# Kernel tuning notes

Measured on AMD Instinct MI355X. Metric: run time of the kernel, lower is better.

The kernel has to match this reference:

```python
import jax, jax.numpy as jnp
import numpy as np

B, C, H, W = 16, 512, 32, 32
NUM_GROUPS = 32
EPS = 1e-5


def setup_inputs() -> dict:
    key = jax.random.key(0)
    ks = jax.random.split(key, 7)
    x = jax.random.normal(ks[0], (B, C, H, W), dtype=jnp.float32)
    gamma = jnp.ones((C,), dtype=jnp.float32)
    beta = jnp.zeros((C,), dtype=jnp.float32)
    # project_in: Conv2d(C, 3C, 1) -> weight [3C, C], bias [3C]
    w_in = jax.random.normal(ks[1], (3 * C, C), dtype=jnp.float32) / np.sqrt(C)
    b_in = jnp.zeros((3 * C,), dtype=jnp.float32)
    # project_out: Conv2d(C, C, 1) with init_scale=0.0 -> zero-init in original;
    # use small random weights so gradients/outputs are non-trivial for testing.
    w_out = jax.random.normal(ks[2], (C, C), dtype=jnp.float32) / np.sqrt(C)
    b_out = jnp.zeros((C,), dtype=jnp.float32)
    return {"x": x, "gamma": gamma, "beta": beta, "w_in": w_in, "b_in": b_in,
            "w_out": w_out, "b_out": b_out}


def group_norm(x, gamma, beta):
    b, c, h, w = x.shape
    xg = x.reshape(b, NUM_GROUPS, c // NUM_GROUPS, h, w)
    mean = xg.mean(axis=(2, 3, 4), keepdims=True)
    var = xg.var(axis=(2, 3, 4), keepdims=True)
    xn = ((xg - mean) * jax.lax.rsqrt(var + EPS)).reshape(b, c, h, w)
    return xn * gamma[None, :, None, None] + beta[None, :, None, None]


def reference(x, gamma, beta, w_in, b_in, w_out, b_out):
    skip = x  # in_channels == out_channels -> Identity skip
    xn = group_norm(x, gamma, beta)
    # 1x1 conv == channel matmul
    qkv = jnp.einsum('oc,bchw->bohw', w_in, xn) + b_in[None, :, None, None]
    q, k, v = jnp.split(qkv, 3, axis=1)  # each [B, C, H, W]
    cm = q.shape[1]
    # [B, H, W, H*W] scores
    scores = jnp.einsum('bchw,bcHW->bhwHW', q, k).reshape(B, H, W, H * W)
    attn = jax.nn.softmax(scores / jnp.sqrt(jnp.float32(cm)), axis=-1)
    attn = attn.reshape(B, H, W, H, W)
    out = jnp.einsum('bhwHW,bcHW->bchw', attn, v)
    out = jnp.einsum('oc,bchw->bohw', w_out, out) + b_out[None, :, None, None]
    return out + skip
```

## Files before the change

### kernel.cpp

```cpp
#include <hip/hip_runtime.h>
#include <hip/hip_bf16.h>
#include <cstdint>
#include <cstddef>

#define HW   1024
#define NC   512
#define NB   16
#define EPSV 1e-5f

typedef __hip_bfloat16 bf16;
typedef __attribute__((ext_vector_type(8))) __bf16 bf16x8;
typedef __attribute__((ext_vector_type(4))) float f32x4;

__device__ __forceinline__ float b2f(bf16 h) { return __bfloat162float(h); }

__device__ __forceinline__ void gload16(const void* g, void* l) {
  __builtin_amdgcn_global_load_lds(
      (const __attribute__((address_space(1))) uint32_t*)g,
      (__attribute__((address_space(3))) uint32_t*)l, 16, 0, 0);
}

__global__ __launch_bounds__(256) void cvt_w_kernel(
    const float* __restrict__ wi, const float* __restrict__ wo,
    bf16* __restrict__ wib, bf16* __restrict__ wob) {
  int i = blockIdx.x * 256 + threadIdx.x;
  const float4* src;
  bf16* dst;
  int j;
  if (i < 196608) { src = (const float4*)wi; j = i; dst = wib; }
  else            { src = (const float4*)wo; j = i - 196608; dst = wob; }
  float4 v = src[j];
  union { bf16 h[4]; uint2 u; } p;
  p.h[0] = __float2bfloat16(v.x); p.h[1] = __float2bfloat16(v.y);
  p.h[2] = __float2bfloat16(v.z); p.h[3] = __float2bfloat16(v.w);
  *(uint2*)&dst[(size_t)j * 4] = p.u;
}

__global__ __launch_bounds__(256) void gn_kernel(
    const float* __restrict__ x, const float* __restrict__ gamma,
    const float* __restrict__ beta, bf16* __restrict__ xn) {
  int blk = blockIdx.x;
  int b = blk >> 5, g = blk & 31;
  size_t base = ((size_t)(b * NC + g * 16)) * HW;
  const float4* src4 = (const float4*)(x + base);
  int t = threadIdx.x;
  float s = 0.f, ss = 0.f;
  float4 v[16];
#pragma unroll
  for (int i = 0; i < 16; ++i) {
    v[i] = src4[t + i * 256];
    s  += v[i].x + v[i].y + v[i].z + v[i].w;
    ss += v[i].x * v[i].x + v[i].y * v[i].y + v[i].z * v[i].z + v[i].w * v[i].w;
  }
  __shared__ float red[256];
  red[t] = s; __syncthreads();
  for (int o = 128; o > 0; o >>= 1) { if (t < o) red[t] += red[t + o]; __syncthreads(); }
  float mean = red[0] * (1.f / 16384.f);
  __syncthreads();
  red[t] = ss; __syncthreads();
  for (int o = 128; o > 0; o >>= 1) { if (t < o) red[t] += red[t + o]; __syncthreads(); }
  float var = red[0] * (1.f / 16384.f) - mean * mean;
  float rstd = rsqrtf(var + EPSV);

  __shared__ bf16 sm[16][1032];
#pragma unroll
  for (int i = 0; i < 16; ++i) {
    int idx = t + i * 256;
    int c = idx >> 8;
    int hw4 = (idx & 255) * 4;
    float gm = gamma[g * 16 + c], bt = beta[g * 16 + c];
    union { bf16 h[4]; uint2 u; } p;
    p.h[0] = __float2bfloat16((v[i].x - mean) * rstd * gm + bt);
    p.h[1] = __float2bfloat16((v[i].y - mean) * rstd * gm + bt);
    p.h[2] = __float2bfloat16((v[i].z - mean) * rstd * gm + bt);
    p.h[3] = __float2bfloat16((v[i].w - mean) * rstd * gm + bt);
    *(uint2*)&sm[c][hw4] = p.u;
  }
  __syncthreads();
  bf16* dst = xn + (size_t)b * HW * NC + g * 16;
#pragma unroll
  for (int it = 0; it < 8; ++it) {
    int u = it * 256 + t;
    int hw = u >> 1;
    int c8 = (u & 1) * 8;
    union { bf16 h[8]; uint4 q; } p;
#pragma unroll
    for (int j = 0; j < 8; ++j) p.h[j] = sm[c8 + j][hw];
    *(uint4*)&dst[(size_t)hw * NC + c8] = p.q;
  }
}

template <int MODE>
__global__ __launch_bounds__(256) void gemm_bt(
    const bf16* __restrict__ A, int lda, long long sA,
    const bf16* __restrict__ B, int ldb, long long sB,
    void* __restrict__ Cv, int ldc, long long sC,
    int K,
    const float* __restrict__ bias) {
  __shared__ bf16 sT[2][128][32];
  int z = blockIdx.z;
  const bf16* Ab = A + (size_t)z * sA;
  const bf16* Bb = B + (size_t)z * sB;
  int n0 = blockIdx.x * 128, m0 = blockIdx.y * 128;
  int t = threadIdx.x;
  int l = t & 63, w = t >> 6;
  int wm = w >> 1, wn = w & 1;

  int srow = t >> 2;
  int scol = (t & 3) * 8;

  f32x4 acc[4][4] = {};

  const bf16* ga0 = Ab + (size_t)(m0 + srow) * lda + scol;
  const bf16* gb0 = Bb + (size_t)(n0 + srow) * ldb + scol;

  for (int k0 = 0; k0 < K; k0 += 32) {
    gload16(ga0 + k0, &sT[0][srow][scol]);
    gload16(ga0 + (size_t)64 * lda + k0, &sT[0][64 + srow][scol]);
    gload16(gb0 + k0, &sT[1][srow][scol]);
    gload16(gb0 + (size_t)64 * ldb + k0, &sT[1][64 + srow][scol]);
    __syncthreads();
    bf16x8 af[4], bfr[4];
    int kc = (l >> 4) * 8;
    int ra = wm * 64 + (l & 15);
    int rb = wn * 64 + (l & 15);
#pragma unroll
    for (int i = 0; i < 4; ++i) {
      af[i]  = *(const bf16x8*)&sT[0][ra + i * 16][kc];
      bfr[i] = *(const bf16x8*)&sT[1][rb + i * 16][kc];
    }
#pragma unroll
    for (int i = 0; i < 4; ++i)
#pragma unroll
      for (int j = 0; j < 4; ++j)
        acc[i][j] = __builtin_amdgcn_mfma_f32_16x16x32_bf16(af[i], bfr[j], acc[i][j], 0, 0, 0);
    __syncthreads();
  }

  int rbase = (l >> 4) * 4;
#pragma unroll
  for (int i = 0; i < 4; ++i) {
    int row = m0 + wm * 64 + i * 16 + rbase;
    float4 bv = make_float4(0.f, 0.f, 0.f, 0.f);
    if (MODE == 0) bv = *(const float4*)&bias[row];
    else if (MODE == 1) { if (bias) bv = *(const float4*)&bias[row]; }
#pragma unroll
    for (int j = 0; j < 4; ++j) {
      int col = n0 + wn * 64 + j * 16 + (l & 15);
      if (MODE == 0) {
        bf16* C = (bf16*)Cv + (size_t)z * sC;
        union { bf16 h[4]; uint2 u; } p;
        p.h[0] = __float2bfloat16(acc[i][j][0] + bv.x);
        p.h[1] = __float2bfloat16(acc[i][j][1] + bv.y);
        p.h[2] = __float2bfloat16(acc[i][j][2] + bv.z);
        p.h[3] = __float2bfloat16(acc[i][j][3] + bv.w);
        *(uint2*)&C[(size_t)col * ldc + row] = p.u;
      } else {
        bf16* C = (bf16*)Cv + (size_t)z * sC;
        float bb[4] = {bv.x, bv.y, bv.z, bv.w};
#pragma unroll
        for (int r = 0; r < 4; ++r)
          C[(size_t)(row + r) * ldc + col] = __float2bfloat16(acc[i][j][r] + bb[r]);
      }
    }
  }
}

__global__ __launch_bounds__(512, 1) void flash_kernel(
    const bf16* __restrict__ qk, const bf16* __restrict__ vcm,
    const bf16* __restrict__ wout, const float* __restrict__ b_out,
    const float* __restrict__ x, float* __restrict__ out) {
  __shared__ char lds[163840];
  char* Qs  = lds;
  char* Kb0 = lds + 65536;
  char* Kb1 = lds + 81920;
  char* Vs  = lds + 98304;
  char* Wb0 = lds + 65536;
  char* Wb1 = lds + 98304;
  float* redl = (float*)(lds + 131072);

  int id = blockIdx.x;
  int xcd = id & 7, rest = id >> 3;
  int q = rest & 15, bh = rest >> 4;
  int b = xcd + bh * 8;
  int i0 = q * 64;

  const char* qkC = (const char*)qk + (size_t)b * 2097152;
  const char* vC  = (const char*)vcm + (size_t)b * 1048576;
  const char* wC  = (const char*)wout;

  int t = threadIdx.x, l = t & 63, w = t >> 6;
  int l15 = l & 15, lq = l >> 4;
  int jg = w >> 1, ih = w & 1;
  int chb = w * 64;

  auto stage_k = [&](int tile_, int c_, char* dst_) {
#pragma unroll
    for (int qq = 0; qq < 2; ++qq) {
      int drow = w * 8 + qq * 4 + lq;
      int cb = l15 * 16;
      gload16(qkC + (size_t)(tile_ * 64 + drow) * 2048 + 1024 + c_ * 256
                  + (cb ^ ((drow & 7) << 4)),
              dst_ + w * 2048 + qq * 1024 + l * 16);
    }
  };
  auto stage_v = [&](int tile_, int v_) {
    int ch = v_ * 64 + w * 8 + (l >> 3);
    int cb = (l & 7) * 16;
    gload16(vC + (size_t)ch * 2048 + tile_ * 128 + (cb ^ ((ch & 7) << 4)),
            Vs + v_ * 8192 + w * 1024 + l * 16);
  };
  auto stage_w = [&](int kc_, char* dst_) {
#pragma unroll
    for (int it = 0; it < 4; ++it) {
      int idx = it * 512 + t;
      int row = idx >> 2, cb = (idx & 3) * 16;
      gload16(wC + (size_t)row * 1024 + kc_ * 64 + (cb ^ ((row & 3) << 4)),
              dst_ + idx * 16);
    }
  };

  {
    const char* qbase = qkC + (size_t)i0 * 2048;
#pragma unroll
    for (int it = 0; it < 8; ++it) {
      int s = it * 8192 + t * 16;
      int i = s >> 10, wb = s & 1023;
      gload16(qbase + (size_t)i * 2048 + (wb ^ ((i & 7) << 4)), Qs + s);
    }
  }
  stage_k(0, 0, Kb0);

  float lacc[2] = {0.f, 0.f};
  f32x4 o[4][4] = {};
  const float scl = 0.044194173824159216f;

  __syncthreads();

  for (int tile = 0; tile < 16; ++tile) {
    char* PsBuf = (tile & 1) ? Kb1 : Kb0;
    f32x4 s[2] = {};
#pragma unroll
    for (int p = 0; p < 4; ++p) {
      if (p < 3) {
        char* kd = ((p + 1 + tile) & 1) ? Kb1 : Kb0;
        stage_k(tile, p + 1, kd);
      }
      stage_v(tile, p * 2);
      stage_v(tile, p * 2 + 1);
      const char* kcur = ((p + tile) & 1) ? Kb1 : Kb0;
      int krow = jg * 16 + l15;
#pragma unroll
      for (int k2 = 0; k2 < 4; ++k2) {
        bf16x8 kf = *(const bf16x8*)(kcur + krow * 256
                      + ((k2 * 64 + lq * 16) ^ ((krow & 7) << 4)));
#pragma unroll
        for (int ni = 0; ni < 2; ++ni) {
          int i = ih * 32 + ni * 16 + l15;
          bf16x8 qf = *(const bf16x8*)(Qs + i * 1024
                        + ((p * 256 + k2 * 64 + lq * 16) ^ ((i & 7) << 4)));
          s[ni] = __builtin_amdgcn_mfma_f32_16x16x32_bf16(kf, qf, s[ni], 0, 0, 0);
        }
      }
      __syncthreads();
    }
#pragma unroll
    for (int ni = 0; ni < 2; ++ni) {
      int i = ih * 32 + ni * 16 + l15;
      float p0 = __expf(s[ni][0] * scl);
      float p1 = __expf(s[ni][1] * scl);
      float p2 = __expf(s[ni][2] * scl);
      float p3 = __expf(s[ni][3] * scl);
      lacc[ni] += p0 + p1 + p2 + p3;
      union { bf16 h[4]; uint64_t u; } pk;
      pk.h[0] = __float2bfloat16(p0); pk.h[1] = __float2bfloat16(p1);
      pk.h[2] = __float2bfloat16(p2); pk.h[3] = __float2bfloat16(p3);
      *(uint64_t*)(PsBuf + i * 128 + ((jg * 32 + lq * 8) ^ ((i & 7) << 4))) = pk.u;
    }
    __syncthreads();
    if (tile < 15) {
      char* kd = ((tile + 1) & 1) ? Kb1 : Kb0;
      stage_k(tile + 1, 0, kd);
    }
#pragma unroll
    for (int ks = 0; ks < 2; ++ks) {
      bf16x8 vf[4];
#pragma unroll
      for (int mi = 0; mi < 4; ++mi) {
        int ch = chb + mi * 16 + l15;
        vf[mi] = *(const bf16x8*)(Vs + ch * 128
                   + ((ks * 64 + lq * 16) ^ ((ch & 7) << 4)));
      }
#pragma unroll
      for (int ni = 0; ni < 4; ++ni) {
        int i = ni * 16 + l15;
        bf16x8 pf = *(const bf16x8*)(PsBuf + i * 128
                      + ((ks * 64 + lq * 16) ^ ((i & 7) << 4)));
#pragma unroll
        for (int mi = 0; mi < 4; ++mi)
          o[mi][ni] = __builtin_amdgcn_mfma_f32_16x16x32_bf16(vf[mi], pf, o[mi][ni], 0, 0, 0);
      }
    }
    __syncthreads();
  }

  stage_w(0, Wb0);
#pragma unroll
  for (int ni = 0; ni < 2; ++ni) {
    float v = lacc[ni];
    v += __shfl_xor(v, 16);
    v += __shfl_xor(v, 32);
    if (l < 16) redl[jg * 64 + ih * 32 + ni * 16 + l] = v;
  }
  __syncthreads();
  float linv[4];
#pragma unroll
  for (int ni = 0; ni < 4; ++ni) {
    int i = ni * 16 + l15;
    linv[ni] = 1.f / (redl[i] + redl[64 + i] + redl[128 + i] + redl[192 + i]);
  }
#pragma unroll
  for (int mi = 0; mi < 4; ++mi)
#pragma unroll
    for (int ni = 0; ni < 4; ++ni) {
      union { bf16 h[4]; uint64_t u; } pk;
#pragma unroll
      for (int r = 0; r < 4; ++r)
        pk.h[r] = __float2bfloat16(o[mi][ni][r] * linv[ni]);
      int i = ni * 16 + l15;
      int c2 = (chb + mi * 16 + lq * 4) * 2;
      *(uint64_t*)(Qs + i * 1024 + (c2 ^ ((i & 7) << 4))) = pk.u;
    }
  __syncthreads();

  f32x4 acc2[4][4] = {};
#pragma unroll
  for (int kc = 0; kc < 16; ++kc) {
    if (kc < 15) stage_w(kc + 1, ((kc + 1) & 1) ? Wb1 : Wb0);
    const char* Wc = (kc & 1) ? Wb1 : Wb0;
    bf16x8 wf[4];
#pragma unroll
    for (int mi = 0; mi < 4; ++mi) {
      int row = chb + mi * 16 + l15;
      wf[mi] = *(const bf16x8*)(Wc + row * 64 + ((lq * 16) ^ ((row & 3) << 4)));
    }
#pragma unroll
    for (int ni = 0; ni < 4; ++ni) {
      int i = ni * 16 + l15;
      bf16x8 pf = *(const bf16x8*)(Qs + i * 1024
                    + ((kc * 64 + lq * 16) ^ ((i & 7) << 4)));
#pragma unroll
      for (int mi = 0; mi < 4; ++mi)
        acc2[mi][ni] = __builtin_amdgcn_mfma_f32_16x16x32_bf16(wf[mi], pf, acc2[mi][ni], 0, 0, 0);
    }
    __syncthreads();
  }

  const float* xb = x + (size_t)b * 524288;
  float* ob = out + (size_t)b * 524288;
#pragma unroll
  for (int mi = 0; mi < 4; ++mi) {
    int cbase = chb + mi * 16 + lq * 4;
    float4 bv = *(const float4*)&b_out[cbase];
    float bb[4] = {bv.x, bv.y, bv.z, bv.w};
#pragma unroll
    for (int ni = 0; ni < 4; ++ni) {
      int i = i0 + ni * 16 + l15;
#pragma unroll
      for (int r = 0; r < 4; ++r) {
        size_t off = (size_t)(cbase + r) * 1024 + i;
        ob[off] = acc2[mi][ni][r] + bb[r] + xb[off];
      }
    }
  }
}

extern "C" void kernel_launch(void* const* d_in, const int* in_sizes, int n_in,
                              void* d_out, int out_size, void* d_ws, size_t ws_size,
                              hipStream_t stream) {
  const float* x     = (const float*)d_in[0];
  const float* gamma = (const float*)d_in[1];
  const float* beta  = (const float*)d_in[2];
  const float* w_in  = (const float*)d_in[3];
  const float* b_in  = (const float*)d_in[4];
  const float* w_out = (const float*)d_in[5];
  const float* b_out = (const float*)d_in[6];
  float* out = (float*)d_out;

  char* w = (char*)d_ws;
  bf16* xn  = (bf16*)w;
  bf16* qk  = (bf16*)(w + ((size_t)16 << 20));
  bf16* vcm = (bf16*)(w + ((size_t)48 << 20));
  bf16* wib = (bf16*)(w + ((size_t)64 << 20));
  bf16* wob = (bf16*)(w + ((size_t)64 << 20) + ((size_t)3 << 19));

  cvt_w_kernel<<<1024, 256, 0, stream>>>(w_in, w_out, wib, wob);
  gn_kernel<<<NB * 32, 256, 0, stream>>>(x, gamma, beta, xn);

  gemm_bt<0><<<dim3(8, 8, NB), 256, 0, stream>>>(
      wib, 512, 0, xn, 512, 512 * 1024, qk, 1024, 1024 * 1024, 512, b_in);
  gemm_bt<1><<<dim3(8, 4, NB), 256, 0, stream>>>(
      wib + 1024 * 512, 512, 0, xn, 512, 512 * 1024, vcm, 1024, 512 * 1024, 512,
      b_in + 1024);

  flash_kernel<<<256, 512, 0, stream>>>(qk, vcm, wob, b_out, x, out);
}
```

Baseline: 146.7 us.

## Re-tile LDS staging into MFMA fragment-major 16x32 blocks instead of XOR swizzle

Changes the LDS layout of the Q, K, V, P and W_out tiles from row-major with XOR swizzling to a fragment-major layout, where each 16-row by 32-element MFMA operand block occupies a contiguous 1 KB region. Global-to-LDS loads are re-addressed to fill this layout, and all MFMA fragment reads become simple linear offsets. The aim is to cut address arithmetic and get conflict-free, contiguous ds_read_b128 accesses. In exchange, each global load now covers only 64-byte row segments, which may reduce global coalescing, and the P and O writes may see different bank-conflict patterns.

```diff
diff --git a/kernel.cpp b/kernel.cpp
--- a/kernel.cpp
+++ b/kernel.cpp
@@ -194,39 +194,37 @@
   int jg = w >> 1, ih = w & 1;
   int chb = w * 64;
 
-  auto stage_k = [&](int tile_, int c_, char* dst_) {
+  auto stage_k = [&](int tile_, int p_, char* dst_) {
 #pragma unroll
     for (int qq = 0; qq < 2; ++qq) {
-      int drow = w * 8 + qq * 4 + lq;
-      int cb = l15 * 16;
-      gload16(qkC + (size_t)(tile_ * 64 + drow) * 2048 + 1024 + c_ * 256
-                  + (cb ^ ((drow & 7) << 4)),
-              dst_ + w * 2048 + qq * 1024 + l * 16);
+      int A = qq * 8192 + t * 16;
+      int jh = A >> 12, k2 = (A >> 10) & 3, jlo = (A >> 6) & 15, cb = A & 63;
+      gload16(qkC + (size_t)(tile_ * 64 + jh * 16 + jlo) * 2048 + 1024
+                  + p_ * 256 + k2 * 64 + cb,
+              dst_ + A);
     }
   };
   auto stage_v = [&](int tile_, int v_) {
-    int ch = v_ * 64 + w * 8 + (l >> 3);
-    int cb = (l & 7) * 16;
-    gload16(vC + (size_t)ch * 2048 + tile_ * 128 + (cb ^ ((ch & 7) << 4)),
-            Vs + v_ * 8192 + w * 1024 + l * 16);
+    int chh = t >> 7, js = (t >> 6) & 1, cl = (t >> 2) & 15, jb = (t & 3) * 16;
+    int ch = v_ * 64 + chh * 16 + cl;
+    gload16(vC + (size_t)ch * 2048 + tile_ * 128 + js * 64 + jb,
+            Vs + v_ * 8192 + t * 16);
   };
   auto stage_w = [&](int kc_, char* dst_) {
 #pragma unroll
     for (int it = 0; it < 4; ++it) {
-      int idx = it * 512 + t;
-      int row = idx >> 2, cb = (idx & 3) * 16;
-      gload16(wC + (size_t)row * 1024 + kc_ * 64 + (cb ^ ((row & 3) << 4)),
-              dst_ + idx * 16);
+      int A = it * 8192 + t * 16;
+      int coh = A >> 10, col = (A >> 6) & 15, cb = A & 63;
+      gload16(wC + (size_t)(coh * 16 + col) * 1024 + kc_ * 64 + cb, dst_ + A);
     }
   };
 
   {
-    const char* qbase = qkC + (size_t)i0 * 2048;
 #pragma unroll
     for (int it = 0; it < 8; ++it) {
-      int s = it * 8192 + t * 16;
-      int i = s >> 10, wb = s & 1023;
-      gload16(qbase + (size_t)i * 2048 + (wb ^ ((i & 7) << 4)), Qs + s);
+      int A = it * 8192 + t * 16;
+      int ih2 = A >> 14, ks = (A >> 10) & 15, ilo = (A >> 6) & 15, cb = A & 63;
+      gload16(qkC + (size_t)(i0 + ih2 * 16 + ilo) * 2048 + ks * 64 + cb, Qs + A);
     }
   }
   stage_k(0, 0, Kb0);
@@ -249,16 +247,13 @@
       stage_v(tile, p * 2);
       stage_v(tile, p * 2 + 1);
       const char* kcur = ((p + tile) & 1) ? Kb1 : Kb0;
-      int krow = jg * 16 + l15;
 #pragma unroll
       for (int k2 = 0; k2 < 4; ++k2) {
-        bf16x8 kf = *(const bf16x8*)(kcur + krow * 256
-                      + ((k2 * 64 + lq * 16) ^ ((krow & 7) << 4)));
+        bf16x8 kf = *(const bf16x8*)(kcur + jg * 4096 + k2 * 1024 + l15 * 64 + lq * 16);
 #pragma unroll
         for (int ni = 0; ni < 2; ++ni) {
-          int i = ih * 32 + ni * 16 + l15;
-          bf16x8 qf = *(const bf16x8*)(Qs + i * 1024
-                        + ((p * 256 + k2 * 64 + lq * 16) ^ ((i & 7) << 4)));
+          bf16x8 qf = *(const bf16x8*)(Qs + (ih * 2 + ni) * 16384
+                        + (p * 4 + k2) * 1024 + l15 * 64 + lq * 16);
           s[ni] = __builtin_amdgcn_mfma_f32_16x16x32_bf16(kf, qf, s[ni], 0, 0, 0);
         }
       }
@@ -275,7 +270,10 @@
       union { bf16 h[4]; uint64_t u; } pk;
       pk.h[0] = __float2bfloat16(p0); pk.h[1] = __float2bfloat16(p1);
       pk.h[2] = __float2bfloat16(p2); pk.h[3] = __float2bfloat16(p3);
-      *(uint64_t*)(PsBuf + i * 128 + ((jg * 32 + lq * 8) ^ ((i & 7) << 4))) = pk.u;
+      int dst = (ih * 2 + ni) * 2048 + (jg >> 1) * 1024 + l15 * 64
+              + (jg & 1) * 32 + lq * 8;
+      *(uint64_t*)(PsBuf + dst) = pk.u;
+      (void)i;
     }
     __syncthreads();
     if (tile < 15) {
@@ -286,16 +284,13 @@
     for (int ks = 0; ks < 2; ++ks) {
       bf16x8 vf[4];
 #pragma unroll
-      for (int mi = 0; mi < 4; ++mi) {
-        int ch = chb + mi * 16 + l15;
-        vf[mi] = *(const bf16x8*)(Vs + ch * 128
-                   + ((ks * 64 + lq * 16) ^ ((ch & 7) << 4)));
-      }
+      for (int mi = 0; mi < 4; ++mi)
+        vf[mi] = *(const bf16x8*)(Vs + (w * 4 + mi) * 2048 + ks * 1024
+                   + l15 * 64 + lq * 16);
 #pragma unroll
       for (int ni = 0; ni < 4; ++ni) {
-        int i = ni * 16 + l15;
-        bf16x8 pf = *(const bf16x8*)(PsBuf + i * 128
-                      + ((ks * 64 + lq * 16) ^ ((i & 7) << 4)));
+        bf16x8 pf = *(const bf16x8*)(PsBuf + ni * 2048 + ks * 1024
+                      + l15 * 64 + lq * 16);
 #pragma unroll
         for (int mi = 0; mi < 4; ++mi)
           o[mi][ni] = __builtin_amdgcn_mfma_f32_16x16x32_bf16(vf[mi], pf, o[mi][ni], 0, 0, 0);
@@ -327,9 +322,9 @@
 #pragma unroll
       for (int r = 0; r < 4; ++r)
         pk.h[r] = __float2bfloat16(o[mi][ni][r] * linv[ni]);
-      int i = ni * 16 + l15;
-      int c2 = (chb + mi * 16 + lq * 4) * 2;
-      *(uint64_t*)(Qs + i * 1024 + (c2 ^ ((i & 7) << 4))) = pk.u;
+      int dst = ni * 16384 + (w * 2 + (mi >> 1)) * 1024 + l15 * 64
+              + (mi & 1) * 32 + lq * 8;
+      *(uint64_t*)(Qs + dst) = pk.u;
     }
   __syncthreads();
 
@@ -340,15 +335,12 @@
     const char* Wc = (kc & 1) ? Wb1 : Wb0;
     bf16x8 wf[4];
 #pragma unroll
-    for (int mi = 0; mi < 4; ++mi) {
-      int row = chb + mi * 16 + l15;
-      wf[mi] = *(const bf16x8*)(Wc + row * 64 + ((lq * 16) ^ ((row & 3) << 4)));
-    }
+    for (int mi = 0; mi < 4; ++mi)
+      wf[mi] = *(const bf16x8*)(Wc + (w * 4 + mi) * 1024 + l15 * 64 + lq * 16);
 #pragma unroll
     for (int ni = 0; ni < 4; ++ni) {
-      int i = ni * 16 + l15;
-      bf16x8 pf = *(const bf16x8*)(Qs + i * 1024
-                    + ((kc * 64 + lq * 16) ^ ((i & 7) << 4)));
+      bf16x8 pf = *(const bf16x8*)(Qs + ni * 16384 + kc * 1024
+                    + l15 * 64 + lq * 16);
 #pragma unroll
       for (int mi = 0; mi < 4; ++mi)
         acc2[mi][ni] = __builtin_amdgcn_mfma_f32_16x16x32_bf16(wf[mi], pf, acc2[mi][ni], 0, 0, 0);
```

New measurement: 151.7 us. 3.4% more time.
